# Optimization experiments

Hardware: AMD Instinct MI355X
Metric: run time of the kernel (lower is better)

## Reference

```python
import math
import jax, jax.numpy as jnp
import numpy as np

HEADS = 8
DIM = 512
HEAD_SIZE = DIM // HEADS  # 64


def setup_inputs() -> dict:
    key = jax.random.key(0)
    ks = jax.random.split(key, 5)
    b, nh, nw, t, d = 16, 16, 16, 16, DIM
    x = jax.random.normal(ks[0], (b, nh, nw, t, d), dtype=jnp.float32)
    s = 1.0 / math.sqrt(d)
    Wq = jax.random.normal(ks[1], (d, d), dtype=jnp.float32) * s
    Wk = jax.random.normal(ks[2], (d, d), dtype=jnp.float32) * s
    Wv = jax.random.normal(ks[3], (d, d), dtype=jnp.float32) * s
    Wo = jax.random.normal(ks[4], (d, d), dtype=jnp.float32) * s
    z = jnp.zeros((d,), dtype=jnp.float32)
    return {"x": x, "Wq": Wq, "bq": z, "Wk": Wk, "bk": z, "Wv": Wv, "bv": z, "Wo": Wo, "bo": z}


def _split_heads(t):
    # [b, n1, n2, T, D] -> [b, n1, n2, H, T, hs]
    b, n1, n2, T, _ = t.shape
    return t.reshape(b, n1, n2, T, HEADS, HEAD_SIZE).transpose(0, 1, 2, 4, 3, 5)


def reference(x, Wq, bq, Wk, bk, Wv, bv, Wo, bo):
    q = _split_heads(x @ Wq + bq)
    k = _split_heads(x @ Wk + bk)
    v = _split_heads(x @ Wv + bv)
    # windowed attention scores: [b, n1, n2, H, T, T]
    scores = jnp.einsum('bnmhtd,bnmhsd->bnmhts', q, k) / math.sqrt(HEAD_SIZE)
    probs = jax.nn.sigmoid(scores)  # NOTE: elementwise sigmoid, not softmax
    ctx = jnp.einsum('bnmhts,bnmhsd->bnmhtd', probs, v)
    b, n1, n2, H, T, hs = ctx.shape
    ctx = ctx.transpose(0, 1, 2, 4, 3, 5).reshape(b, n1, n2, T, H * hs)
    return ctx @ Wo + bo
```

## Files before the change

kernel.cpp:

```cpp
#include <hip/hip_runtime.h>
#include <hip/hip_bf16.h>

typedef float f32x4 __attribute__((ext_vector_type(4)));
typedef __bf16 bf16x8 __attribute__((ext_vector_type(8)));
typedef unsigned short u16x4 __attribute__((ext_vector_type(4)));
typedef unsigned short u16x8 __attribute__((ext_vector_type(8)));

__device__ __forceinline__ unsigned short f2bf(float f) {
  union { float f; unsigned u; } x; x.f = f;
  unsigned r = x.u + 0x7FFFu + ((x.u >> 16) & 1u);
  return (unsigned short)(r >> 16);
}
__device__ __forceinline__ float bf2f(unsigned short u) {
  union { unsigned u; float f; } x; x.u = ((unsigned)u) << 16;
  return x.f;
}

__device__ __forceinline__ void gl16(const void* g, void* l) {
  __builtin_amdgcn_global_load_lds(
      (const __attribute__((address_space(1))) unsigned*)g,
      (__attribute__((address_space(3))) unsigned*)l, 16, 0, 0);
}

__global__ __launch_bounds__(256) void prep_wt(const float* __restrict__ Wq,
                                               const float* __restrict__ Wk,
                                               const float* __restrict__ Wv,
                                               const float* __restrict__ Wo,
                                               unsigned short* __restrict__ WT) {
  __shared__ unsigned short ts[64][65];
  const float* W = (blockIdx.z == 0) ? Wq : (blockIdx.z == 1) ? Wk
                   : (blockIdx.z == 2) ? Wv : Wo;
  const int t = threadIdx.x;
  const int kbase = blockIdx.y * 64;
  const int nbase = blockIdx.x * 64;
  for (int i = 0; i < 16; ++i) {
    int idx = i * 256 + t;
    int r = idx >> 6, c = idx & 63;
    ts[r][c] = f2bf(W[(size_t)(kbase + r) * 512 + nbase + c]);
  }
  __syncthreads();
  unsigned short* dst = WT + (size_t)blockIdx.z * 512 * 512;
  for (int i = 0; i < 16; ++i) {
    int idx = i * 256 + t;
    int nn = idx >> 6, kk = idx & 63;
    dst[(size_t)(nbase + nn) * 512 + kbase + kk] = ts[kk][nn];
  }
}

__global__ void prep_bias(const float* __restrict__ bq, const float* __restrict__ bk,
                          const float* __restrict__ bv, float* __restrict__ biasc) {
  int i = blockIdx.x * 256 + threadIdx.x;
  if (i < 512) biasc[i] = bq[i];
  else if (i < 1024) biasc[i] = bk[i - 512];
  else if (i < 1536) biasc[i] = bv[i - 1024];
}

__global__ __launch_bounds__(256) void convert_x(const float* __restrict__ x,
                                                 unsigned short* __restrict__ xb,
                                                 long long n8) {
  long long i = (long long)blockIdx.x * 256 + threadIdx.x;
  const long long stride = (long long)gridDim.x * 256;
  for (; i < n8; i += stride) {
    f32x4 a = *reinterpret_cast<const f32x4*>(&x[i * 8]);
    f32x4 b = *reinterpret_cast<const f32x4*>(&x[i * 8 + 4]);
    u16x8 o;
    o[0] = f2bf(a[0]); o[1] = f2bf(a[1]); o[2] = f2bf(a[2]); o[3] = f2bf(a[3]);
    o[4] = f2bf(b[0]); o[5] = f2bf(b[1]); o[6] = f2bf(b[2]); o[7] = f2bf(b[3]);
    *reinterpret_cast<u16x8*>(&xb[i * 8]) = o;
  }
}

template <typename CT>
__global__ __launch_bounds__(256) void gemm_glds(
    const unsigned short* __restrict__ A, int lda,
    const unsigned short* __restrict__ BT,
    CT* __restrict__ C, int ldc,
    const float* __restrict__ bias, int NB) {
  __shared__ alignas(16) unsigned short As[128 * 64];
  __shared__ alignas(16) unsigned short Bs[128 * 64];
  const int t = threadIdx.x;
  const int lane = t & 63;
  const int w = t >> 6;
  const int wm = w >> 1, wn = w & 1;

  const int nwg = gridDim.x;
  const int cpx = nwg >> 3;
  const int wg = (blockIdx.x & 7) * cpx + (blockIdx.x >> 3);
  const int n0 = (wg % NB) * 128;
  const int m0 = (wg / NB) * 128;

  const int l8 = lane >> 3, l7 = lane & 7;
  const unsigned short* ga = A + (size_t)(m0 + w * 32 + l8) * lda + ((l7 ^ l8) << 3);
  const unsigned short* gb = BT + (size_t)(n0 + w * 32 + l8) * 512 + ((l7 ^ l8) << 3);
  unsigned short* lA = &As[(w * 32) * 64];
  unsigned short* lB = &Bs[(w * 32) * 64];

  f32x4 acc[4][4];
#pragma unroll
  for (int i = 0; i < 4; ++i)
#pragma unroll
    for (int j = 0; j < 4; ++j) acc[i][j] = (f32x4){0.f, 0.f, 0.f, 0.f};

  for (int k0 = 0; k0 < 512; k0 += 64) {
#pragma unroll
    for (int i = 0; i < 4; ++i) {
      gl16(ga + (size_t)i * 8 * lda, lA + i * 8 * 64);
      gl16(gb + (size_t)i * 8 * 512, lB + i * 8 * 64);
    }
    ga += 64;
    gb += 64;
    __syncthreads();
#pragma unroll
    for (int kf = 0; kf < 2; ++kf) {
      bf16x8 af[4], bg[4];
#pragma unroll
      for (int mi = 0; mi < 4; ++mi) {
        int row = wm * 64 + mi * 16 + (lane & 15);
        int cb = (kf * 64 + ((lane >> 4) << 4)) ^ (l7 << 4);
        af[mi] = *reinterpret_cast<const bf16x8*>(&As[row * 64 + (cb >> 1)]);
      }
#pragma unroll
      for (int ni = 0; ni < 4; ++ni) {
        int row = wn * 64 + ni * 16 + (lane & 15);
        int cb = (kf * 64 + ((lane >> 4) << 4)) ^ (l7 << 4);
        bg[ni] = *reinterpret_cast<const bf16x8*>(&Bs[row * 64 + (cb >> 1)]);
      }
#pragma unroll
      for (int mi = 0; mi < 4; ++mi)
#pragma unroll
        for (int ni = 0; ni < 4; ++ni)
          acc[mi][ni] = __builtin_amdgcn_mfma_f32_16x16x32_bf16(af[mi], bg[ni], acc[mi][ni], 0, 0, 0);
    }
    __syncthreads();
  }

#pragma unroll
  for (int ni = 0; ni < 4; ++ni) {
    int col = n0 + wn * 64 + ni * 16 + (lane & 15);
    float bc = bias ? bias[col] : 0.0f;
#pragma unroll
    for (int mi = 0; mi < 4; ++mi) {
      int rowb = m0 + wm * 64 + mi * 16 + ((lane >> 4) << 2);
#pragma unroll
      for (int r = 0; r < 4; ++r) {
        float v = acc[mi][ni][r] + bc;
        if constexpr (sizeof(CT) == 2)
          C[(size_t)(rowb + r) * ldc + col] = (CT)f2bf(v);
        else
          C[(size_t)(rowb + r) * ldc + col] = (CT)v;
      }
    }
  }
}

__global__ __launch_bounds__(256) void attn_kernel(unsigned short* __restrict__ QKV) {
  __shared__ alignas(16) unsigned short qs[16][1544];
  __shared__ unsigned short ps[8][16][16];
  const int t = threadIdx.x;
  const size_t base = (size_t)blockIdx.x * 16;

  {
    int row = t >> 4;
    int cb = (t & 15) * 96;
    const unsigned short* src = QKV + (base + row) * 1536;
#pragma unroll
    for (int i = 0; i < 24; ++i) {
      int c = cb + i * 4;
      *reinterpret_cast<u16x4*>(&qs[row][c]) = *reinterpret_cast<const u16x4*>(&src[c]);
    }
  }
  __syncthreads();

  const int tq = t >> 4;
  const int tk = t & 15;
#pragma unroll
  for (int h = 0; h < 8; ++h) {
    float acc = 0.f;
#pragma unroll
    for (int dc = 0; dc < 64; dc += 8) {
      u16x8 q8 = *reinterpret_cast<const u16x8*>(&qs[tq][h * 64 + dc]);
      u16x8 k8 = *reinterpret_cast<const u16x8*>(&qs[tk][512 + h * 64 + dc]);
#pragma unroll
      for (int j = 0; j < 8; ++j) acc += bf2f(q8[j]) * bf2f(k8[j]);
    }
    ps[h][tq][tk] = f2bf(1.0f / (1.0f + __expf(-acc * 0.125f)));
  }
  __syncthreads();

  const int row = t >> 4;
  const int cb4 = (t & 15) * 4;
  unsigned short* dst = QKV + (base + row) * 1536 + 1024;
#pragma unroll
  for (int h = 0; h < 8; ++h) {
    f32x4 acc = (f32x4){0.f, 0.f, 0.f, 0.f};
#pragma unroll
    for (int s = 0; s < 16; ++s) {
      float p = bf2f(ps[h][row][s]);
      u16x4 v4 = *reinterpret_cast<const u16x4*>(&qs[s][1024 + h * 64 + cb4]);
      acc[0] += p * bf2f(v4[0]); acc[1] += p * bf2f(v4[1]);
      acc[2] += p * bf2f(v4[2]); acc[3] += p * bf2f(v4[3]);
    }
    u16x4 o4;
    o4[0] = f2bf(acc[0]); o4[1] = f2bf(acc[1]); o4[2] = f2bf(acc[2]); o4[3] = f2bf(acc[3]);
    *reinterpret_cast<u16x4*>(&dst[h * 64 + cb4]) = o4;
  }
}

extern "C" void kernel_launch(void* const* d_in, const int* in_sizes, int n_in,
                              void* d_out, int out_size, void* d_ws, size_t ws_size,
                              hipStream_t stream) {
  const float* x  = (const float*)d_in[0];
  const float* Wq = (const float*)d_in[1];
  const float* bq = (const float*)d_in[2];
  const float* Wk = (const float*)d_in[3];
  const float* bk = (const float*)d_in[4];
  const float* Wv = (const float*)d_in[5];
  const float* bv = (const float*)d_in[6];
  const float* Wo = (const float*)d_in[7];
  const float* bo = (const float*)d_in[8];
  float* out = (float*)d_out;

  const int M = 65536;
  char* ws = (char*)d_ws;
  unsigned short* WT = (unsigned short*)ws;
  float* biasc = (float*)(ws + (size_t)2048 * 512 * 2);
  const long long prep_bytes = (long long)2048 * 512 * 2 + 8192;

  prep_wt<<<dim3(8, 8, 4), 256, 0, stream>>>(Wq, Wk, Wv, Wo, WT);
  prep_bias<<<6, 256, 0, stream>>>(bq, bk, bv, biasc);

  long long avail = (long long)ws_size - prep_bytes;
  int chunk_rows = 65536;
  while (chunk_rows > 1024 && (long long)chunk_rows * 4096 > avail) chunk_rows >>= 1;
  const int nchunks = M / chunk_rows;

  unsigned short* Xb  = (unsigned short*)(ws + prep_bytes);
  unsigned short* QKV = Xb + (size_t)chunk_rows * 512;

  for (int c = 0; c < nchunks; ++c) {
    const size_t row0 = (size_t)c * chunk_rows;
    convert_x<<<2048, 256, 0, stream>>>(x + row0 * 512, Xb,
                                        (long long)chunk_rows * 64);
    gemm_glds<unsigned short><<<(chunk_rows / 128) * 12, 256, 0, stream>>>(
        Xb, 512, WT, QKV, 1536, biasc, 12);
    attn_kernel<<<chunk_rows / 16, 256, 0, stream>>>(QKV);
    gemm_glds<float><<<(chunk_rows / 128) * 4, 256, 0, stream>>>(
        QKV + 1024, 1536, WT + (size_t)1536 * 512, out + row0 * 512, 512, bo, 4);
  }
}
```

Measured before the change: 360.1 us.

## Replace 128x128 GEMM with 256x256 double-buffered pipelined MFMA kernel

Replaces the single-buffered 128x128-tile GEMM with a 512-thread, 256x256-tile kernel. It double-buffers the LDS tiles and interleaves the async global-to-LDS loads of the next K-tile with the MFMA phases of the current one, using explicit vmcnt waits, barriers and setprio. The larger tile raises arithmetic intensity per loaded byte, and the software pipeline hides memory latency behind compute. In exchange it uses 128KB of LDS per block and many more accumulator registers, which limits occupancy. It also removes the null-bias check and requires chunk sizes that are multiples of 256 rows.

```diff
diff --git a/kernel.cpp b/kernel.cpp
--- a/kernel.cpp
+++ b/kernel.cpp
@@ -71,76 +71,120 @@
 }
 
 template <typename CT>
-__global__ __launch_bounds__(256) void gemm_glds(
+__global__ __launch_bounds__(512, 2) void gemm256(
     const unsigned short* __restrict__ A, int lda,
     const unsigned short* __restrict__ BT,
     CT* __restrict__ C, int ldc,
     const float* __restrict__ bias, int NB) {
-  __shared__ alignas(16) unsigned short As[128 * 64];
-  __shared__ alignas(16) unsigned short Bs[128 * 64];
+  __shared__ alignas(16) unsigned short As[2][16384];
+  __shared__ alignas(16) unsigned short Bs[2][16384];
   const int t = threadIdx.x;
   const int lane = t & 63;
   const int w = t >> 6;
-  const int wm = w >> 1, wn = w & 1;
+  const int wm = w >> 2, wn = w & 3;
 
   const int nwg = gridDim.x;
   const int cpx = nwg >> 3;
   const int wg = (blockIdx.x & 7) * cpx + (blockIdx.x >> 3);
-  const int n0 = (wg % NB) * 128;
-  const int m0 = (wg / NB) * 128;
-
-  const int l8 = lane >> 3, l7 = lane & 7;
-  const unsigned short* ga = A + (size_t)(m0 + w * 32 + l8) * lda + ((l7 ^ l8) << 3);
-  const unsigned short* gb = BT + (size_t)(n0 + w * 32 + l8) * 512 + ((l7 ^ l8) << 3);
-  unsigned short* lA = &As[(w * 32) * 64];
-  unsigned short* lB = &Bs[(w * 32) * 64];
-
-  f32x4 acc[4][4];
-#pragma unroll
-  for (int i = 0; i < 4; ++i)
+  const int n0 = (wg % NB) * 256;
+  const int m0 = (wg / NB) * 256;
+
+  const int sr = lane >> 3;
+  const int sg = ((lane & 7) ^ sr) << 3;
+  const unsigned short* gA = A + (size_t)(m0 + w * 8 + sr) * lda + sg;
+  const unsigned short* gB = BT + (size_t)(n0 + w * 8 + sr) * 512 + sg;
+  const int lw = w * 512;
+
+#define STAGE_A(kt, h, b)                                                   \
+  { const unsigned short* g_ = gA + (size_t)(h) * 128 * lda + (kt) * 64;    \
+    unsigned short* l_ = &As[b][(h) * 8192 + lw];                           \
+    gl16(g_, l_); gl16(g_ + (size_t)64 * lda, l_ + 4096); }
+#define STAGE_B(kt, h, b)                                                   \
+  { const unsigned short* g_ = gB + (size_t)(h) * 128 * 512 + (kt) * 64;    \
+    unsigned short* l_ = &Bs[b][(h) * 8192 + lw];                           \
+    gl16(g_, l_); gl16(g_ + (size_t)64 * 512, l_ + 4096); }
+
+  const int fr = lane & 15;
+  const int fg = lane >> 4;
+  const int fx = lane & 7;
+  auto readA = [&](int b, int mi, int kf) -> bf16x8 {
+    return *reinterpret_cast<const bf16x8*>(
+        &As[b][(wm * 128 + mi * 16 + fr) * 64 + ((((kf << 2) + fg) ^ fx) << 3)]);
+  };
+  auto readB = [&](int b, int ni, int kf) -> bf16x8 {
+    return *reinterpret_cast<const bf16x8*>(
+        &Bs[b][(wn * 64 + ni * 16 + fr) * 64 + ((((kf << 2) + fg) ^ fx) << 3)]);
+  };
+
+  f32x4 acc[8][4];
+#pragma unroll
+  for (int i = 0; i < 8; ++i)
 #pragma unroll
     for (int j = 0; j < 4; ++j) acc[i][j] = (f32x4){0.f, 0.f, 0.f, 0.f};
-
-  for (int k0 = 0; k0 < 512; k0 += 64) {
-#pragma unroll
-    for (int i = 0; i < 4; ++i) {
-      gl16(ga + (size_t)i * 8 * lda, lA + i * 8 * 64);
-      gl16(gb + (size_t)i * 8 * 512, lB + i * 8 * 64);
-    }
-    ga += 64;
-    gb += 64;
-    __syncthreads();
-#pragma unroll
-    for (int kf = 0; kf < 2; ++kf) {
-      bf16x8 af[4], bg[4];
-#pragma unroll
-      for (int mi = 0; mi < 4; ++mi) {
-        int row = wm * 64 + mi * 16 + (lane & 15);
-        int cb = (kf * 64 + ((lane >> 4) << 4)) ^ (l7 << 4);
-        af[mi] = *reinterpret_cast<const bf16x8*>(&As[row * 64 + (cb >> 1)]);
-      }
-#pragma unroll
-      for (int ni = 0; ni < 4; ++ni) {
-        int row = wn * 64 + ni * 16 + (lane & 15);
-        int cb = (kf * 64 + ((lane >> 4) << 4)) ^ (l7 << 4);
-        bg[ni] = *reinterpret_cast<const bf16x8*>(&Bs[row * 64 + (cb >> 1)]);
-      }
-#pragma unroll
-      for (int mi = 0; mi < 4; ++mi)
-#pragma unroll
-        for (int ni = 0; ni < 4; ++ni)
-          acc[mi][ni] = __builtin_amdgcn_mfma_f32_16x16x32_bf16(af[mi], bg[ni], acc[mi][ni], 0, 0, 0);
-    }
-    __syncthreads();
-  }
+  bf16x8 bfr[4][2];
+
+#define PHASE(b, q, READB, STAGES, VM)                                       \
+  {                                                                          \
+    bf16x8 a0_ = readA(b, 2 * (q), 0), a1_ = readA(b, 2 * (q), 1);           \
+    bf16x8 a2_ = readA(b, 2 * (q) + 1, 0), a3_ = readA(b, 2 * (q) + 1, 1);   \
+    if (READB) {                                                             \
+      _Pragma("unroll") for (int ni = 0; ni < 4; ++ni) {                     \
+        bfr[ni][0] = readB(b, ni, 0);                                        \
+        bfr[ni][1] = readB(b, ni, 1);                                        \
+      }                                                                      \
+    }                                                                        \
+    STAGES;                                                                  \
+    if ((VM) == 4) asm volatile("s_waitcnt vmcnt(4)" ::: "memory");          \
+    if ((VM) == 0) asm volatile("s_waitcnt vmcnt(0)" ::: "memory");          \
+    __builtin_amdgcn_s_barrier();                                            \
+    asm volatile("s_waitcnt lgkmcnt(0)" ::: "memory");                       \
+    __builtin_amdgcn_sched_barrier(0);                                       \
+    __builtin_amdgcn_s_setprio(1);                                           \
+    _Pragma("unroll") for (int ni = 0; ni < 4; ++ni) {                       \
+      acc[2 * (q)][ni] = __builtin_amdgcn_mfma_f32_16x16x32_bf16(            \
+          a0_, bfr[ni][0], acc[2 * (q)][ni], 0, 0, 0);                       \
+      acc[2 * (q)][ni] = __builtin_amdgcn_mfma_f32_16x16x32_bf16(            \
+          a1_, bfr[ni][1], acc[2 * (q)][ni], 0, 0, 0);                       \
+      acc[2 * (q) + 1][ni] = __builtin_amdgcn_mfma_f32_16x16x32_bf16(        \
+          a2_, bfr[ni][0], acc[2 * (q) + 1][ni], 0, 0, 0);                   \
+      acc[2 * (q) + 1][ni] = __builtin_amdgcn_mfma_f32_16x16x32_bf16(        \
+          a3_, bfr[ni][1], acc[2 * (q) + 1][ni], 0, 0, 0);                   \
+    }                                                                        \
+    __builtin_amdgcn_s_setprio(0);                                           \
+    __builtin_amdgcn_s_barrier();                                            \
+  }
+
+  STAGE_B(0, 0, 0); STAGE_B(0, 1, 0);
+  STAGE_A(0, 0, 0); STAGE_A(0, 1, 0);
+  STAGE_B(1, 0, 1); STAGE_B(1, 1, 1);
+  asm volatile("s_waitcnt vmcnt(4)" ::: "memory");
+  __builtin_amdgcn_s_barrier();
+
+#pragma unroll
+  for (int i = 0; i < 4; ++i) {
+    const bool s2 = (i < 3);
+    const int vmA = s2 ? 4 : 0;
+    const int vmB = s2 ? 4 : 0;
+    PHASE(0, 0, true,  { STAGE_A(2 * i + 1, 0, 1) }, -1);
+    PHASE(0, 1, false, { STAGE_A(2 * i + 1, 1, 1) if (s2) STAGE_B(2 * i + 2, 0, 0) }, -1);
+    PHASE(0, 2, false, { if (s2) STAGE_B(2 * i + 2, 1, 0) }, -1);
+    PHASE(0, 3, false, {}, vmA);
+    PHASE(1, 0, true,  { if (s2) STAGE_A(2 * i + 2, 0, 0) }, -1);
+    PHASE(1, 1, false, { if (s2) STAGE_A(2 * i + 2, 1, 0) }, -1);
+    PHASE(1, 2, false, { if (s2) STAGE_B(2 * i + 3, 0, 1) }, -1);
+    PHASE(1, 3, false, { if (s2) STAGE_B(2 * i + 3, 1, 1) }, vmB);
+  }
+#undef PHASE
+#undef STAGE_A
+#undef STAGE_B
 
 #pragma unroll
   for (int ni = 0; ni < 4; ++ni) {
-    int col = n0 + wn * 64 + ni * 16 + (lane & 15);
-    float bc = bias ? bias[col] : 0.0f;
-#pragma unroll
-    for (int mi = 0; mi < 4; ++mi) {
-      int rowb = m0 + wm * 64 + mi * 16 + ((lane >> 4) << 2);
+    int col = n0 + wn * 64 + ni * 16 + fr;
+    float bc = bias[col];
+#pragma unroll
+    for (int mi = 0; mi < 8; ++mi) {
+      int rowb = m0 + wm * 128 + mi * 16 + fg * 4;
 #pragma unroll
       for (int r = 0; r < 4; ++r) {
         float v = acc[mi][ni][r] + bc;
@@ -231,7 +275,7 @@
 
   long long avail = (long long)ws_size - prep_bytes;
   int chunk_rows = 65536;
-  while (chunk_rows > 1024 && (long long)chunk_rows * 4096 > avail) chunk_rows >>= 1;
+  while (chunk_rows > 2048 && (long long)chunk_rows * 4096 > avail) chunk_rows >>= 1;
   const int nchunks = M / chunk_rows;
 
   unsigned short* Xb  = (unsigned short*)(ws + prep_bytes);
@@ -239,12 +283,13 @@
 
   for (int c = 0; c < nchunks; ++c) {
     const size_t row0 = (size_t)c * chunk_rows;
+    const int mt = chunk_rows / 256;
     convert_x<<<2048, 256, 0, stream>>>(x + row0 * 512, Xb,
                                         (long long)chunk_rows * 64);
-    gemm_glds<unsigned short><<<(chunk_rows / 128) * 12, 256, 0, stream>>>(
-        Xb, 512, WT, QKV, 1536, biasc, 12);
+    gemm256<unsigned short><<<mt * 6, 512, 0, stream>>>(
+        Xb, 512, WT, QKV, 1536, biasc, 6);
     attn_kernel<<<chunk_rows / 16, 256, 0, stream>>>(QKV);
-    gemm_glds<float><<<(chunk_rows / 128) * 4, 256, 0, stream>>>(
-        QKV + 1024, 1536, WT + (size_t)1536 * 512, out + row0 * 512, 512, bo, 4);
-  }
-}
+    gemm256<float><<<mt * 2, 512, 0, stream>>>(
+        QKV + 1024, 1536, WT + (size_t)1536 * 512, out + row0 * 512, 512, bo, 2);
+  }
+}
```

After: 340.7 us. 1.06x faster.
